# Optimization experiments

Measured on AMD Instinct MI355X. Metric: run time of the kernel, lower is better.

The kernel has to match this reference:

```python
import jax, jax.numpy as jnp
import numpy as np


def _ste_sign(x):
    # Binarize to {-1, +1} (sign with sign(0)=+1), straight-through estimator:
    # forward value is sign(x), gradient passes through identity (matches the
    # torch .data-swap trick where autograd sees the fp parameter).
    s = jnp.where(x >= 0, 1.0, -1.0).astype(x.dtype)
    return x + jax.lax.stop_gradient(s - x)


def setup_inputs() -> dict:
    key = jax.random.key(0)
    k1, k2, k3 = jax.random.split(key, 3)
    N, IN, OUT = 8192, 4096, 4096
    x = jax.random.normal(k1, (N, IN), dtype=jnp.float32)
    fp_weight = jax.random.normal(k2, (OUT, IN), dtype=jnp.float32) * 0.02
    bound = 1.0 / np.sqrt(IN)
    fp_bias = jax.random.uniform(k3, (OUT,), dtype=jnp.float32, minval=-bound, maxval=bound)
    return {"x": x, "fp_weight": fp_weight, "fp_bias": fp_bias}


def reference(x, fp_weight, fp_bias):
    # BinarizedLinear forward (training / use_bnn_origin_eval path):
    #   input  -> binarize_tensor (sign quantization to +-1)
    #   weight -> binarize_tensor (sign quantization to +-1)
    #   output = F.linear(bin_input, bin_weight) + bias
    bx = _ste_sign(x)                      # [N, IN]
    bw = _ste_sign(fp_weight)              # [OUT, IN]
    out = jnp.einsum('ni,oi->no', bx, bw)  # [N, OUT]
    out = out + fp_bias[None, :]
    return out
```

## Files before the change

kernel.cpp:

```cpp
#include <hip/hip_runtime.h>
#include <stdint.h>

#define NROW 8192
#define KDIM 4096
#define NOUT 4096

typedef __attribute__((ext_vector_type(4))) int i32x4;

__global__ __launch_bounds__(256)
void bin_i8_fused(const float* __restrict__ x, const float* __restrict__ w,
                  uint32_t* __restrict__ xq, uint32_t* __restrict__ wq,
                  int n4x, int n4tot) {
    int i = blockIdx.x * blockDim.x + threadIdx.x;
    const int stride = gridDim.x * blockDim.x;
    for (; i < n4tot; i += stride) {
        const float4* src;
        uint32_t* dst;
        int j;
        if (i < n4x) { src = (const float4*)x; dst = xq; j = i; }
        else         { src = (const float4*)w; dst = wq; j = i - n4x; }
        float4 v = src[j];
        uint32_t b0 = (v.x < 0.0f) ? 0xFFu : 0x01u;
        uint32_t b1 = (v.y < 0.0f) ? 0xFFu : 0x01u;
        uint32_t b2 = (v.z < 0.0f) ? 0xFFu : 0x01u;
        uint32_t b3 = (v.w < 0.0f) ? 0xFFu : 0x01u;
        dst[j] = b0 | (b1 << 8) | (b2 << 16) | (b3 << 24);
    }
}

#define BM 128
#define BN 128
#define BK 64

__device__ __forceinline__ void gload_lds16(const void* g, void* l) {
    __builtin_amdgcn_global_load_lds(
        (const __attribute__((address_space(1))) uint32_t*)g,
        (__attribute__((address_space(3))) uint32_t*)l, 16, 0, 0);
}

__global__ __launch_bounds__(256)
void i8_mfma_gemm(const uint8_t* __restrict__ xq, const uint8_t* __restrict__ wq,
                  const float* __restrict__ bias, float* __restrict__ out) {
    __shared__ __align__(16) uint8_t As[2][BM][BK];
    __shared__ __align__(16) uint8_t Bs[2][BN][BK];

    const int tid  = threadIdx.x;
    const int wid  = tid >> 6;
    const int lane = tid & 63;
    const int wr   = wid >> 1;
    const int wc   = wid & 1;
    const int row0 = blockIdx.y * BM;
    const int col0 = blockIdx.x * BN;

    const int c0 = wid * 64 + lane;
    const int c1 = 256 + wid * 64 + lane;
    const int r0 = c0 >> 2, k0 = ((c0 & 3) ^ ((c0 >> 3) & 3)) * 16;
    const int r1 = c1 >> 2, k1 = ((c1 & 3) ^ ((c1 >> 3) & 3)) * 16;

    const uint8_t* gA0 = xq + (size_t)(row0 + r0) * KDIM + k0;
    const uint8_t* gA1 = xq + (size_t)(row0 + r1) * KDIM + k1;
    const uint8_t* gB0 = wq + (size_t)(col0 + r0) * KDIM + k0;
    const uint8_t* gB1 = wq + (size_t)(col0 + r1) * KDIM + k1;

    i32x4 acc[4][4];
#pragma unroll
    for (int m = 0; m < 4; ++m)
#pragma unroll
        for (int n = 0; n < 4; ++n) acc[m][n] = (i32x4){0, 0, 0, 0};

    const int g    = lane >> 4;
    const int lr   = lane & 15;
    const int swzk = (g ^ ((lr >> 1) & 3)) * 16;

    {
        uint8_t* la = &As[0][0][0];
        uint8_t* lb = &Bs[0][0][0];
        gload_lds16(gA0, la + c0 * 16);
        gload_lds16(gA1, la + c1 * 16);
        gload_lds16(gB0, lb + c0 * 16);
        gload_lds16(gB1, lb + c1 * 16);
    }

    int cur = 0;
    for (int kb = 0; kb < KDIM; kb += BK) {
        __syncthreads();

        if (kb + BK < KDIM) {
            const int nxt = cur ^ 1;
            uint8_t* la = &As[nxt][0][0];
            uint8_t* lb = &Bs[nxt][0][0];
            const int ko = kb + BK;
            gload_lds16(gA0 + ko, la + c0 * 16);
            gload_lds16(gA1 + ko, la + c1 * 16);
            gload_lds16(gB0 + ko, lb + c0 * 16);
            gload_lds16(gB1 + ko, lb + c1 * 16);
        }

        i32x4 af[4], bf[4];
#pragma unroll
        for (int m = 0; m < 4; ++m)
            af[m] = *(const i32x4*)&As[cur][wr * 64 + m * 16 + lr][swzk];
#pragma unroll
        for (int n = 0; n < 4; ++n)
            bf[n] = *(const i32x4*)&Bs[cur][wc * 64 + n * 16 + lr][swzk];

#pragma unroll
        for (int m = 0; m < 4; ++m)
#pragma unroll
            for (int n = 0; n < 4; ++n)
                acc[m][n] = __builtin_amdgcn_mfma_i32_16x16x64_i8(
                    af[m], bf[n], acc[m][n], 0, 0, 0);

        cur ^= 1;
    }

#pragma unroll
    for (int n = 0; n < 4; ++n) {
        const int col = col0 + wc * 64 + n * 16 + lr;
        const float bv = bias[col];
#pragma unroll
        for (int m = 0; m < 4; ++m) {
            const int rbase = row0 + wr * 64 + m * 16 + g * 4;
#pragma unroll
            for (int r = 0; r < 4; ++r)
                out[(size_t)(rbase + r) * NOUT + col] = (float)acc[m][n][r] + bv;
        }
    }
}

extern "C" void kernel_launch(void* const* d_in, const int* in_sizes, int n_in,
                              void* d_out, int out_size, void* d_ws, size_t ws_size,
                              hipStream_t stream) {
    const float* x = (const float*)d_in[0];
    const float* w = (const float*)d_in[1];
    const float* b = (const float*)d_in[2];
    float* out = (float*)d_out;

    uint8_t* xq = (uint8_t*)d_ws;
    uint8_t* wq = xq + (size_t)NROW * KDIM;
    (void)ws_size;

    const int n4x = NROW * KDIM / 4;
    const int n4t = n4x + NOUT * KDIM / 4;
    bin_i8_fused<<<3072, 256, 0, stream>>>(x, w, (uint32_t*)xq, (uint32_t*)wq,
                                           n4x, n4t);

    dim3 grid(NOUT / BN, NROW / BM);
    i8_mfma_gemm<<<grid, 256, 0, stream>>>(xq, wq, b, out);
}
```

Baseline: 434.1 us.

## Enlarge GEMM tile to 256x256 with 8 waves and interleaved staged pipeline

Moves the int8 MFMA GEMM from 128x128 tiles with 4 waves to 256x256 tiles with 8 waves and a K step of 128, split into two 64-wide halves. Global-to-LDS loads of the next stage are spread across four compute phases, with explicit vmcnt waits, barriers and s_setprio around the MFMA clusters. The aim is more data reuse per LDS byte and better overlap of memory with matrix math. In exchange it raises register and LDS pressure (128KB LDS per block) and fits fewer blocks on the grid.

```diff
diff --git a/kernel.cpp b/kernel.cpp
--- a/kernel.cpp
+++ b/kernel.cpp
@@ -28,9 +28,10 @@
     }
 }
 
-#define BM 128
-#define BN 128
-#define BK 64
+#define BM 256
+#define BN 256
+#define BKB 128
+#define NT (KDIM / BKB)
 
 __device__ __forceinline__ void gload_lds16(const void* g, void* l) {
     __builtin_amdgcn_global_load_lds(
@@ -38,92 +39,149 @@
         (__attribute__((address_space(3))) uint32_t*)l, 16, 0, 0);
 }
 
-__global__ __launch_bounds__(256)
+__global__ __launch_bounds__(512, 2)
 void i8_mfma_gemm(const uint8_t* __restrict__ xq, const uint8_t* __restrict__ wq,
                   const float* __restrict__ bias, float* __restrict__ out) {
-    __shared__ __align__(16) uint8_t As[2][BM][BK];
-    __shared__ __align__(16) uint8_t Bs[2][BN][BK];
+    __shared__ __align__(16) uint8_t As[2][2][256][64];
+    __shared__ __align__(16) uint8_t Bs[2][2][256][64];
 
     const int tid  = threadIdx.x;
     const int wid  = tid >> 6;
     const int lane = tid & 63;
-    const int wr   = wid >> 1;
-    const int wc   = wid & 1;
+    const int wr   = wid >> 2;
+    const int wc   = wid & 3;
+    const int lr   = lane & 15;
+    const int g    = lane >> 4;
     const int row0 = blockIdx.y * BM;
     const int col0 = blockIdx.x * BN;
 
     const int c0 = wid * 64 + lane;
-    const int c1 = 256 + wid * 64 + lane;
-    const int r0 = c0 >> 2, k0 = ((c0 & 3) ^ ((c0 >> 3) & 3)) * 16;
-    const int r1 = c1 >> 2, k1 = ((c1 & 3) ^ ((c1 >> 3) & 3)) * 16;
-
-    const uint8_t* gA0 = xq + (size_t)(row0 + r0) * KDIM + k0;
-    const uint8_t* gA1 = xq + (size_t)(row0 + r1) * KDIM + k1;
-    const uint8_t* gB0 = wq + (size_t)(col0 + r0) * KDIM + k0;
-    const uint8_t* gB1 = wq + (size_t)(col0 + r1) * KDIM + k1;
-
-    i32x4 acc[4][4];
-#pragma unroll
-    for (int m = 0; m < 4; ++m)
+    const int c1 = 512 + c0;
+    const int r0 = c0 >> 2, s0 = ((c0 & 3) ^ (r0 & 3)) * 16;
+    const int r1 = c1 >> 2, s1 = ((c1 & 3) ^ (r1 & 3)) * 16;
+
+    const uint8_t* gA0 = xq + (size_t)(row0 + r0) * KDIM + s0;
+    const uint8_t* gA1 = xq + (size_t)(row0 + r1) * KDIM + s1;
+    const uint8_t* gB0 = wq + (size_t)(col0 + r0) * KDIM + s0;
+    const uint8_t* gB1 = wq + (size_t)(col0 + r1) * KDIM + s1;
+
+    const int sread = (g ^ (lr & 3)) * 16;
+    const int ra = wr * 128 + lr;
+    const int cb = wc * 64 + lr;
+
+#define STAGE_A(sd, kh, ko) do {                                  \
+        uint8_t* _l = &As[sd][kh][0][0];                          \
+        gload_lds16(gA0 + (ko) + (kh) * 64, _l + c0 * 16);        \
+        gload_lds16(gA1 + (ko) + (kh) * 64, _l + c1 * 16);        \
+    } while (0)
+#define STAGE_B(sd, kh, ko) do {                                  \
+        uint8_t* _l = &Bs[sd][kh][0][0];                          \
+        gload_lds16(gB0 + (ko) + (kh) * 64, _l + c0 * 16);        \
+        gload_lds16(gB1 + (ko) + (kh) * 64, _l + c1 * 16);        \
+    } while (0)
+
+    i32x4 acc[8][4];
+#pragma unroll
+    for (int m = 0; m < 8; ++m)
 #pragma unroll
         for (int n = 0; n < 4; ++n) acc[m][n] = (i32x4){0, 0, 0, 0};
 
-    const int g    = lane >> 4;
-    const int lr   = lane & 15;
-    const int swzk = (g ^ ((lr >> 1) & 3)) * 16;
-
-    {
-        uint8_t* la = &As[0][0][0];
-        uint8_t* lb = &Bs[0][0][0];
-        gload_lds16(gA0, la + c0 * 16);
-        gload_lds16(gA1, la + c1 * 16);
-        gload_lds16(gB0, lb + c0 * 16);
-        gload_lds16(gB1, lb + c1 * 16);
+    STAGE_A(0, 0, 0);
+    STAGE_B(0, 0, 0);
+    STAGE_A(0, 1, 0);
+    STAGE_B(0, 1, 0);
+    asm volatile("s_waitcnt vmcnt(4)" ::: "memory");
+    __builtin_amdgcn_s_barrier();
+
+#pragma unroll 1
+    for (int t = 0; t < NT; ++t) {
+        const int d  = t & 1;
+        const int sd = d ^ 1;
+        const int ko = (t + 1 < NT ? t + 1 : t) * BKB;
+
+        i32x4 a0[4], a1[4], b0[4], b1[4];
+
+#pragma unroll
+        for (int m = 0; m < 4; ++m)
+            a0[m] = *(const i32x4*)&As[d][0][ra + m * 16][sread];
+#pragma unroll
+        for (int n = 0; n < 4; ++n)
+            b0[n] = *(const i32x4*)&Bs[d][0][cb + n * 16][sread];
+        STAGE_A(sd, 0, ko);
+        __builtin_amdgcn_s_barrier();
+        __builtin_amdgcn_s_setprio(1);
+#pragma unroll
+        for (int m = 0; m < 4; ++m)
+#pragma unroll
+            for (int n = 0; n < 4; ++n)
+                acc[m][n] = __builtin_amdgcn_mfma_i32_16x16x64_i8(
+                    a0[m], b0[n], acc[m][n], 0, 0, 0);
+        __builtin_amdgcn_s_setprio(0);
+        __builtin_amdgcn_s_barrier();
+
+#pragma unroll
+        for (int m = 0; m < 4; ++m)
+            a1[m] = *(const i32x4*)&As[d][0][ra + 64 + m * 16][sread];
+        STAGE_B(sd, 0, ko);
+        asm volatile("s_waitcnt vmcnt(4)" ::: "memory");
+        __builtin_amdgcn_s_barrier();
+        __builtin_amdgcn_s_setprio(1);
+#pragma unroll
+        for (int m = 0; m < 4; ++m)
+#pragma unroll
+            for (int n = 0; n < 4; ++n)
+                acc[4 + m][n] = __builtin_amdgcn_mfma_i32_16x16x64_i8(
+                    a1[m], b0[n], acc[4 + m][n], 0, 0, 0);
+        __builtin_amdgcn_s_setprio(0);
+        __builtin_amdgcn_s_barrier();
+
+#pragma unroll
+        for (int m = 0; m < 4; ++m)
+            a0[m] = *(const i32x4*)&As[d][1][ra + m * 16][sread];
+#pragma unroll
+        for (int n = 0; n < 4; ++n)
+            b1[n] = *(const i32x4*)&Bs[d][1][cb + n * 16][sread];
+        STAGE_A(sd, 1, ko);
+        __builtin_amdgcn_s_barrier();
+        __builtin_amdgcn_s_setprio(1);
+#pragma unroll
+        for (int m = 0; m < 4; ++m)
+#pragma unroll
+            for (int n = 0; n < 4; ++n)
+                acc[m][n] = __builtin_amdgcn_mfma_i32_16x16x64_i8(
+                    a0[m], b1[n], acc[m][n], 0, 0, 0);
+        __builtin_amdgcn_s_setprio(0);
+        __builtin_amdgcn_s_barrier();
+
+#pragma unroll
+        for (int m = 0; m < 4; ++m)
+            a1[m] = *(const i32x4*)&As[d][1][ra + 64 + m * 16][sread];
+        STAGE_B(sd, 1, ko);
+        asm volatile("s_waitcnt vmcnt(4)" ::: "memory");
+        __builtin_amdgcn_s_barrier();
+        __builtin_amdgcn_s_setprio(1);
+#pragma unroll
+        for (int m = 0; m < 4; ++m)
+#pragma unroll
+            for (int n = 0; n < 4; ++n)
+                acc[4 + m][n] = __builtin_amdgcn_mfma_i32_16x16x64_i8(
+                    a1[m], b1[n], acc[4 + m][n], 0, 0, 0);
+        __builtin_amdgcn_s_setprio(0);
+        __builtin_amdgcn_s_barrier();
     }
-
-    int cur = 0;
-    for (int kb = 0; kb < KDIM; kb += BK) {
-        __syncthreads();
-
-        if (kb + BK < KDIM) {
-            const int nxt = cur ^ 1;
-            uint8_t* la = &As[nxt][0][0];
-            uint8_t* lb = &Bs[nxt][0][0];
-            const int ko = kb + BK;
-            gload_lds16(gA0 + ko, la + c0 * 16);
-            gload_lds16(gA1 + ko, la + c1 * 16);
-            gload_lds16(gB0 + ko, lb + c0 * 16);
-            gload_lds16(gB1 + ko, lb + c1 * 16);
-        }
-
-        i32x4 af[4], bf[4];
-#pragma unroll
-        for (int m = 0; m < 4; ++m)
-            af[m] = *(const i32x4*)&As[cur][wr * 64 + m * 16 + lr][swzk];
-#pragma unroll
-        for (int n = 0; n < 4; ++n)
-            bf[n] = *(const i32x4*)&Bs[cur][wc * 64 + n * 16 + lr][swzk];
-
-#pragma unroll
-        for (int m = 0; m < 4; ++m)
-#pragma unroll
-            for (int n = 0; n < 4; ++n)
-                acc[m][n] = __builtin_amdgcn_mfma_i32_16x16x64_i8(
-                    af[m], bf[n], acc[m][n], 0, 0, 0);
-
-        cur ^= 1;
-    }
+#undef STAGE_A
+#undef STAGE_B
 
 #pragma unroll
     for (int n = 0; n < 4; ++n) {
         const int col = col0 + wc * 64 + n * 16 + lr;
         const float bv = bias[col];
 #pragma unroll
-        for (int m = 0; m < 4; ++m) {
-            const int rbase = row0 + wr * 64 + m * 16 + g * 4;
+        for (int m = 0; m < 8; ++m) {
+            const int rb = row0 + wr * 128 + m * 16 + g * 4;
 #pragma unroll
             for (int r = 0; r < 4; ++r)
-                out[(size_t)(rbase + r) * NOUT + col] = (float)acc[m][n][r] + bv;
+                out[(size_t)(rb + r) * NOUT + col] = (float)acc[m][n][r] + bv;
         }
     }
 }
@@ -146,5 +204,5 @@
                                            n4x, n4t);
 
     dim3 grid(NOUT / BN, NROW / BM);
-    i8_mfma_gemm<<<grid, 256, 0, stream>>>(xq, wq, b, out);
-}
+    i8_mfma_gemm<<<grid, 512, 0, stream>>>(xq, wq, b, out);
+}
```

Measured after the change: 432.1 us. No clear change (-0.5%).

## Enlarge int8 GEMM tile to 256x256 with 4-stage LDS pipeline

Applied to the files above, without the earlier changes.

Grows the int8 MFMA GEMM block tile from 128x128 to 256x256 and uses 512 threads, each wave computing a 128x64 sub-tile. The aim is more data reuse per LDS byte and less global traffic. The LDS double buffer becomes a 4-slot ring with prefetch distance 2, a vmcnt wait and a single barrier per K step, replacing the syncthreads-per-iteration scheme. MFMA sections also get raised wave priority. Each block now uses 128KB of LDS, so it likely fits only one block per CU despite the launch bound of 2. It also needs more accumulator registers.

```diff
diff --git a/kernel.cpp b/kernel.cpp
--- a/kernel.cpp
+++ b/kernel.cpp
@@ -28,9 +28,10 @@
     }
 }
 
-#define BM 128
-#define BN 128
-#define BK 64
+#define BM 256
+#define BN 256
+#define BKB 64
+#define NT (KDIM / BKB)
 
 __device__ __forceinline__ void gload_lds16(const void* g, void* l) {
     __builtin_amdgcn_global_load_lds(
@@ -38,92 +39,97 @@
         (__attribute__((address_space(3))) uint32_t*)l, 16, 0, 0);
 }
 
-__global__ __launch_bounds__(256)
+__global__ __launch_bounds__(512, 2)
 void i8_mfma_gemm(const uint8_t* __restrict__ xq, const uint8_t* __restrict__ wq,
                   const float* __restrict__ bias, float* __restrict__ out) {
-    __shared__ __align__(16) uint8_t As[2][BM][BK];
-    __shared__ __align__(16) uint8_t Bs[2][BN][BK];
+    __shared__ __align__(16) uint8_t As[4][256][64];
+    __shared__ __align__(16) uint8_t Bs[4][256][64];
 
     const int tid  = threadIdx.x;
     const int wid  = tid >> 6;
     const int lane = tid & 63;
-    const int wr   = wid >> 1;
-    const int wc   = wid & 1;
+    const int wr   = wid >> 2;
+    const int wc   = wid & 3;
+    const int lr   = lane & 15;
+    const int g    = lane >> 4;
     const int row0 = blockIdx.y * BM;
     const int col0 = blockIdx.x * BN;
 
     const int c0 = wid * 64 + lane;
-    const int c1 = 256 + wid * 64 + lane;
-    const int r0 = c0 >> 2, k0 = ((c0 & 3) ^ ((c0 >> 3) & 3)) * 16;
-    const int r1 = c1 >> 2, k1 = ((c1 & 3) ^ ((c1 >> 3) & 3)) * 16;
+    const int c1 = 512 + c0;
+    const int s0 = (((c0 & 3) ^ ((c0 >> 3) & 3))) * 16;
+    const int s1 = (((c1 & 3) ^ ((c1 >> 3) & 3))) * 16;
+    const int r0 = c0 >> 2;
+    const int r1 = c1 >> 2;
 
-    const uint8_t* gA0 = xq + (size_t)(row0 + r0) * KDIM + k0;
-    const uint8_t* gA1 = xq + (size_t)(row0 + r1) * KDIM + k1;
-    const uint8_t* gB0 = wq + (size_t)(col0 + r0) * KDIM + k0;
-    const uint8_t* gB1 = wq + (size_t)(col0 + r1) * KDIM + k1;
+    const uint8_t* gA0 = xq + (size_t)(row0 + r0) * KDIM + s0;
+    const uint8_t* gA1 = xq + (size_t)(row0 + r1) * KDIM + s1;
+    const uint8_t* gB0 = wq + (size_t)(col0 + r0) * KDIM + s0;
+    const uint8_t* gB1 = wq + (size_t)(col0 + r1) * KDIM + s1;
 
-    i32x4 acc[4][4];
+    const int sread = (g ^ ((lr >> 1) & 3)) * 16;
+    const int ra = wr * 128 + lr;
+    const int cb = wc * 64 + lr;
+
+#define STAGE(sb, ko) do {                                        \
+        uint8_t* _la = &As[sb][0][0];                             \
+        uint8_t* _lb = &Bs[sb][0][0];                             \
+        gload_lds16(gA0 + (ko), _la + c0 * 16);                   \
+        gload_lds16(gA1 + (ko), _la + c1 * 16);                   \
+        gload_lds16(gB0 + (ko), _lb + c0 * 16);                   \
+        gload_lds16(gB1 + (ko), _lb + c1 * 16);                   \
+    } while (0)
+#define FENCE() asm volatile("" ::: "memory")
+
+    i32x4 acc[8][4];
 #pragma unroll
-    for (int m = 0; m < 4; ++m)
+    for (int m = 0; m < 8; ++m)
 #pragma unroll
         for (int n = 0; n < 4; ++n) acc[m][n] = (i32x4){0, 0, 0, 0};
 
-    const int g    = lane >> 4;
-    const int lr   = lane & 15;
-    const int swzk = (g ^ ((lr >> 1) & 3)) * 16;
+    STAGE(0, 0);
+    STAGE(1, BKB);
 
-    {
-        uint8_t* la = &As[0][0][0];
-        uint8_t* lb = &Bs[0][0][0];
-        gload_lds16(gA0, la + c0 * 16);
-        gload_lds16(gA1, la + c1 * 16);
-        gload_lds16(gB0, lb + c0 * 16);
-        gload_lds16(gB1, lb + c1 * 16);
-    }
+#pragma unroll 1
+    for (int t = 0; t < NT; ++t) {
+        const int rb = t & 3;
+        const int sb = (t + 2) & 3;
+        const int ko = (t + 2 < NT ? t + 2 : NT - 1) * BKB;
 
-    int cur = 0;
-    for (int kb = 0; kb < KDIM; kb += BK) {
-        __syncthreads();
+        STAGE(sb, ko);
+        asm volatile("s_waitcnt vmcnt(8)" ::: "memory");
+        __builtin_amdgcn_s_barrier();
+        FENCE();
 
-        if (kb + BK < KDIM) {
-            const int nxt = cur ^ 1;
-            uint8_t* la = &As[nxt][0][0];
-            uint8_t* lb = &Bs[nxt][0][0];
-            const int ko = kb + BK;
-            gload_lds16(gA0 + ko, la + c0 * 16);
-            gload_lds16(gA1 + ko, la + c1 * 16);
-            gload_lds16(gB0 + ko, lb + c0 * 16);
-            gload_lds16(gB1 + ko, lb + c1 * 16);
-        }
-
-        i32x4 af[4], bf[4];
+        i32x4 af[8], bf[4];
 #pragma unroll
-        for (int m = 0; m < 4; ++m)
-            af[m] = *(const i32x4*)&As[cur][wr * 64 + m * 16 + lr][swzk];
+        for (int m = 0; m < 8; ++m)
+            af[m] = *(const i32x4*)&As[rb][ra + m * 16][sread];
 #pragma unroll
         for (int n = 0; n < 4; ++n)
-            bf[n] = *(const i32x4*)&Bs[cur][wc * 64 + n * 16 + lr][swzk];
+            bf[n] = *(const i32x4*)&Bs[rb][cb + n * 16][sread];
 
+        __builtin_amdgcn_s_setprio(1);
 #pragma unroll
-        for (int m = 0; m < 4; ++m)
+        for (int m = 0; m < 8; ++m)
 #pragma unroll
             for (int n = 0; n < 4; ++n)
                 acc[m][n] = __builtin_amdgcn_mfma_i32_16x16x64_i8(
                     af[m], bf[n], acc[m][n], 0, 0, 0);
-
-        cur ^= 1;
+        __builtin_amdgcn_s_setprio(0);
     }
+#undef STAGE
 
 #pragma unroll
     for (int n = 0; n < 4; ++n) {
         const int col = col0 + wc * 64 + n * 16 + lr;
         const float bv = bias[col];
 #pragma unroll
-        for (int m = 0; m < 4; ++m) {
-            const int rbase = row0 + wr * 64 + m * 16 + g * 4;
+        for (int m = 0; m < 8; ++m) {
+            const int rb2 = row0 + wr * 128 + m * 16 + g * 4;
 #pragma unroll
             for (int r = 0; r < 4; ++r)
-                out[(size_t)(rbase + r) * NOUT + col] = (float)acc[m][n][r] + bv;
+                out[(size_t)(rb2 + r) * NOUT + col] = (float)acc[m][n][r] + bv;
         }
     }
 }
@@ -146,5 +152,5 @@
                                            n4x, n4t);
 
     dim3 grid(NOUT / BN, NROW / BM);
-    i8_mfma_gemm<<<grid, 256, 0, stream>>>(xq, wq, b, out);
+    i8_mfma_gemm<<<grid, 512, 0, stream>>>(xq, wq, b, out);
 }
```

Result: faster. 403.7 us (-7.0%).
